# Performance work log

Hardware: AMD Instinct MI355X
Metric: run time of the kernel (lower is better)

Reference implementation:

```python
import math
import jax, jax.numpy as jnp
import numpy as np

B = 1024
D = 384
Q = 65536
TOPK = 128
HARD_W = 2.0
TEMP_START = 0.2
TEMP_END = 0.05
WARMUP = 10


def _temperature(epoch):
    # curriculum cosine decay (epoch is a Python int)
    if epoch >= WARMUP:
        return TEMP_END
    progress = epoch / max(1, WARMUP)
    return TEMP_END + 0.5 * (TEMP_START - TEMP_END) * (1.0 + math.cos(math.pi * progress))


def _normalize(x):
    # F.normalize: x / max(||x||, eps)
    n = jnp.linalg.norm(x, axis=-1, keepdims=True)
    return x / jnp.maximum(n, 1e-12)


def _hard_neg_reweight(logits):
    # logits: [B, N]; labels = arange(B) (diagonal positives)
    b = logits.shape[0]
    rows = jnp.arange(b)
    neg_logits = logits.at[rows, rows].set(-jnp.inf)      # mask positives
    _, hard_idx = jax.lax.top_k(neg_logits, TOPK)          # [B, TOPK] hardest negatives
    weights = jnp.ones_like(logits)
    weights = weights.at[rows[:, None], hard_idx].set(HARD_W)
    weights = weights.at[rows, rows].set(1.0)
    return logits * weights


def _cross_entropy_diag(logits):
    b = logits.shape[0]
    logp = jax.nn.log_softmax(logits, axis=-1)
    return -jnp.mean(logp[jnp.arange(b), jnp.arange(b)])


def setup_inputs() -> dict:
    key = jax.random.key(0)
    k1, k2, k3, k4 = jax.random.split(key, 4)
    rgb_feat = jax.random.normal(k1, (B, D), dtype=jnp.float32)
    ir_feat = jax.random.normal(k2, (B, D), dtype=jnp.float32)
    rgb_queue = _normalize(jax.random.normal(k3, (Q, D), dtype=jnp.float32))
    ir_queue = _normalize(jax.random.normal(k4, (Q, D), dtype=jnp.float32))
    return {"rgb_feat": rgb_feat, "ir_feat": ir_feat,
            "rgb_queue": rgb_queue, "ir_queue": ir_queue, "epoch": 0}


def reference(rgb_feat, ir_feat, rgb_queue, ir_queue, epoch):
    temp = _temperature(epoch)
    rgb_z = _normalize(rgb_feat.astype(jnp.float32))
    ir_z = _normalize(ir_feat.astype(jnp.float32))
    ir_all = jnp.concatenate([ir_z, ir_queue], axis=0)    # [B+Q, D]
    rgb_all = jnp.concatenate([rgb_z, rgb_queue], axis=0)
    logits_r2i = (rgb_z @ ir_all.T) / temp                # [B, B+Q]
    logits_i2r = (ir_z @ rgb_all.T) / temp
    logits_r2i = _hard_neg_reweight(logits_r2i)
    logits_i2r = _hard_neg_reweight(logits_i2r)
    return 0.5 * (_cross_entropy_diag(logits_r2i) + _cross_entropy_diag(logits_i2r))
```

## Files before the change

### kernel.cpp

```cpp
#include <hip/hip_runtime.h>
#include <hip/hip_bf16.h>

#define B_    1024
#define D_    384
#define Q_    65536
#define N_    66560
#define TOPK_ 128

#define NBIN_ 4096
#define CAP_  2048

typedef __bf16 bf16x8 __attribute__((ext_vector_type(8)));
typedef float  f32x4  __attribute__((ext_vector_type(4)));
typedef unsigned short u16;
typedef u16 u16x8 __attribute__((ext_vector_type(8)));

__device__ __forceinline__ unsigned short f2bf(float x) {
  unsigned int u = __float_as_uint(x);
  unsigned int r = (u + 0x7fffu + ((u >> 16) & 1u)) >> 16;
  return (unsigned short)r;
}

__device__ __forceinline__ void gld_lds16(const void* g, void* l) {
  __builtin_amdgcn_global_load_lds(
      (__attribute__((address_space(1))) void*)(g),
      (__attribute__((address_space(3))) void*)(l), 16, 0, 0);
}

__device__ __forceinline__ unsigned int bf2key(unsigned int u) {
  return u ^ ((u & 0x8000u) ? 0xFFFFu : 0x8000u);
}

__global__ __launch_bounds__(64) void k_normalize(
    const float* __restrict__ rgb, const float* __restrict__ ir,
    const int* __restrict__ ep,
    u16* __restrict__ zrA, u16* __restrict__ ziA,
    u16* __restrict__ zrU, u16* __restrict__ ziU)
{
  int r = blockIdx.x & (B_ - 1);
  bool isIr = blockIdx.x >= B_;
  const float* src = (isIr ? ir : rgb) + (size_t)r * D_;
  u16* dA = (isIr ? ziA : zrA) + (size_t)r * D_;
  u16* dU = (isIr ? ziU : zrU) + (size_t)r * D_;
  int t = threadIdx.x;
  float x[6]; float ss = 0.f;
  #pragma unroll
  for (int k = 0; k < 6; ++k) { x[k] = src[t + 64*k]; ss += x[k]*x[k]; }
  #pragma unroll
  for (int off = 32; off > 0; off >>= 1) ss += __shfl_down(ss, off);
  ss = __shfl(ss, 0);
  float inv = 1.0f / fmaxf(sqrtf(ss), 1e-12f);

  int e = ep[0];
  float temp;
  if (e >= 10) temp = 0.05f;
  else {
    float p = (float)e * 0.1f;
    temp = 0.05f + 0.075f * (1.0f + cosf(3.14159265358979323846f * p));
  }
  float itemp = 1.0f / temp;

  #pragma unroll
  for (int k = 0; k < 6; ++k) {
    float z = x[k] * inv;
    dU[t + 64*k] = f2bf(z);
    dA[t + 64*k] = f2bf(z * itemp);
  }
}

__global__ __launch_bounds__(256) void k_build_ball(
    const u16* __restrict__ zU, const float* __restrict__ queue,
    u16* __restrict__ ball)
{
  size_t i = ((size_t)blockIdx.x * 256 + threadIdx.x) * 8;
  const size_t zElems = (size_t)B_ * D_;
  if (i < zElems) {
    *(uint4*)(ball + i) = *(const uint4*)(zU + i);
  } else {
    const float* q = queue + (i - zElems);
    float4 a = *(const float4*)q;
    float4 b = *(const float4*)(q + 4);
    u16x8 o;
    o[0] = f2bf(a.x); o[1] = f2bf(a.y); o[2] = f2bf(a.z); o[3] = f2bf(a.w);
    o[4] = f2bf(b.x); o[5] = f2bf(b.y); o[6] = f2bf(b.z); o[7] = f2bf(b.w);
    *(u16x8*)(ball + i) = o;
  }
}

#define BK_ 64
__global__ __launch_bounds__(256) void k_gemm(
    const u16* __restrict__ A,
    const u16* __restrict__ ball,
    u16* __restrict__ C,
    float* __restrict__ diag,
    int r0, int mtiles)
{
  __shared__ u16 As[128 * BK_];
  __shared__ u16 Bs[128 * BK_];

  int bid = blockIdx.x;
  int nwg = gridDim.x;
  int cpx = nwg >> 3;
  int wgid = (bid & 7) * cpx + (bid >> 3);
  int nt = wgid / mtiles;
  int mt = wgid - nt * mtiles;

  const int tid  = threadIdx.x;
  const int wave = tid >> 6, lane = tid & 63;
  const int wm = wave >> 1, wn = wave & 1;
  const int mbase = mt * 128;
  const int nbase = nt * 128;
  const u16* Ab = A    + (size_t)(r0 + mbase) * D_;
  const u16* Bb = ball + (size_t)nbase * D_;

  f32x4 acc[4][4];
  #pragma unroll
  for (int m = 0; m < 4; ++m)
    #pragma unroll
    for (int n = 0; n < 4; ++n)
      #pragma unroll
      for (int r = 0; r < 4; ++r) acc[m][n][r] = 0.0f;

  for (int ks = 0; ks < D_; ks += BK_) {
    #pragma unroll
    for (int i = 0; i < 4; ++i) {
      int f = i * 256 + tid;
      int rr = f >> 3, c = f & 7;
      int koff = (((c * 16) ^ ((rr & 7) << 4)) >> 1);
      const u16* ga = Ab + (size_t)rr * D_ + ks + koff;
      const u16* gb = Bb + (size_t)rr * D_ + ks + koff;
      u16* la = As + (size_t)(i * 256 + wave * 64) * 8;
      u16* lb = Bs + (size_t)(i * 256 + wave * 64) * 8;
      gld_lds16(ga, la);
      gld_lds16(gb, lb);
    }
    __syncthreads();

    const int lr = lane & 15, lk = (lane >> 4) * 8;
    #pragma unroll
    for (int kk = 0; kk < BK_; kk += 32) {
      bf16x8 af[4], bq[4];
      const int kb = (kk + lk) * 2;
      #pragma unroll
      for (int m = 0; m < 4; ++m) {
        int row = wm*64 + m*16 + lr;
        af[m] = *(const bf16x8*)((const char*)As + row * 128 + (kb ^ ((row & 7) << 4)));
      }
      #pragma unroll
      for (int n = 0; n < 4; ++n) {
        int row = wn*64 + n*16 + lr;
        bq[n] = *(const bf16x8*)((const char*)Bs + row * 128 + (kb ^ ((row & 7) << 4)));
      }
      #pragma unroll
      for (int m = 0; m < 4; ++m)
        #pragma unroll
        for (int n = 0; n < 4; ++n)
          acc[m][n] = __builtin_amdgcn_mfma_f32_16x16x32_bf16(af[m], bq[n], acc[m][n], 0, 0, 0);
    }
    __syncthreads();
  }

  const int lr = lane & 15;
  const int rowq = (lane >> 4) * 4;
  #pragma unroll
  for (int m = 0; m < 4; ++m) {
    #pragma unroll
    for (int n = 0; n < 4; ++n) {
      int col = nbase + wn*64 + n*16 + lr;
      #pragma unroll
      for (int r = 0; r < 4; ++r) {
        int srow = mbase + wm*64 + m*16 + rowq + r;
        float x = acc[m][n][r];
        int grow = r0 + srow;
        if (col == grow) { diag[grow] = x; x = -60.0f; }
        C[(size_t)srow * N_ + col] = f2bf(x);
      }
    }
  }
}

__global__ __launch_bounds__(256) void k_select(
    const u16* __restrict__ C, const float* __restrict__ diag,
    float* __restrict__ rowloss, int r0)
{
  __shared__ unsigned int hist[NBIN_];
  __shared__ float vals[CAP_];
  __shared__ float fred[256];
  __shared__ unsigned int csum[256];
  __shared__ int sh_bstar, sh_above, sh_cnt;

  const int t = threadIdx.x;
  const int grow = r0 + blockIdx.x;
  const u16x8* p = (const u16x8*)(C + (size_t)blockIdx.x * N_);

  uint4* h4 = (uint4*)hist;
  #pragma unroll
  for (int i = 0; i < 4; ++i) h4[i * 256 + t] = make_uint4(0,0,0,0);
  if (t == 0) sh_cnt = 0;
  __syncthreads();

  float es0 = 0.f, es1 = 0.f;
  #pragma unroll 1
  for (int base = 0; base < 8192; base += 2048) {
    u16x8 v[8];
    #pragma unroll
    for (int j = 0; j < 8; ++j) v[j] = p[base + j * 256 + t];
    #pragma unroll
    for (int j = 0; j < 8; ++j) {
      #pragma unroll
      for (int e = 0; e < 8; ++e) {
        unsigned int u = (unsigned int)(unsigned short)v[j][e];
        atomicAdd(&hist[bf2key(u) >> 4], 1u);
        float ex = __expf(__uint_as_float(u << 16));
        if (j & 1) es1 += ex; else es0 += ex;
      }
    }
  }
  if (t < 128) {
    u16x8 v = p[8192 + t];
    #pragma unroll
    for (int e = 0; e < 8; ++e) {
      unsigned int u = (unsigned int)(unsigned short)v[e];
      atomicAdd(&hist[bf2key(u) >> 4], 1u);
      es0 += __expf(__uint_as_float(u << 16));
    }
  }
  float esum = es0 + es1;
  __syncthreads();

  unsigned int S = 0;
  #pragma unroll
  for (int i = 0; i < 16; ++i) S += hist[t * 16 + i];
  csum[t] = S;
  __syncthreads();

  unsigned int a = S;
  #pragma unroll
  for (int s = 1; s < 256; s <<= 1) {
    unsigned int add = (t + s < 256) ? csum[t + s] : 0u;
    __syncthreads();
    a += add; csum[t] = a;
    __syncthreads();
  }

  int above_chunk = (t < 255) ? (int)csum[t + 1] : 0;
  if (above_chunk < TOPK_ && above_chunk + (int)S >= TOPK_) {
    int cum = above_chunk;
    #pragma unroll 1
    for (int i = 15; i >= 0; --i) {
      int c = (int)hist[t * 16 + i];
      if (cum + c >= TOPK_) { sh_bstar = t * 16 + i; sh_above = cum; break; }
      cum += c;
    }
  }
  __syncthreads();
  const unsigned int bstar = (unsigned int)sh_bstar;
  const int A = sh_above;

  float delta = 0.f;
  #pragma unroll 1
  for (int base = 0; base < 8192; base += 2048) {
    u16x8 v[8];
    #pragma unroll
    for (int j = 0; j < 8; ++j) v[j] = p[base + j * 256 + t];
    #pragma unroll
    for (int j = 0; j < 8; ++j) {
      #pragma unroll
      for (int e = 0; e < 8; ++e) {
        unsigned int u = (unsigned int)(unsigned short)v[j][e];
        unsigned int bin = bf2key(u) >> 4;
        if (bin >= bstar) {
          float val = __uint_as_float(u << 16);
          if (bin > bstar) delta += __expf(2.f * val) - __expf(val);
          else { int s = atomicAdd(&sh_cnt, 1); if (s < CAP_) vals[s] = val; }
        }
      }
    }
  }
  if (t < 128) {
    u16x8 v = p[8192 + t];
    #pragma unroll
    for (int e = 0; e < 8; ++e) {
      unsigned int u = (unsigned int)(unsigned short)v[e];
      unsigned int bin = bf2key(u) >> 4;
      if (bin >= bstar) {
        float val = __uint_as_float(u << 16);
        if (bin > bstar) delta += __expf(2.f * val) - __expf(val);
        else { int s = atomicAdd(&sh_cnt, 1); if (s < CAP_) vals[s] = val; }
      }
    }
  }
  __syncthreads();

  int C2 = sh_cnt < CAP_ ? sh_cnt : CAP_;
  int need = TOPK_ - A;
  for (int i = t; i < C2; i += 256) {
    float v = vals[i];
    int g = 0;
    for (int k = 0; k < C2; ++k)
      g += (vals[k] > v) || (vals[k] == v && k < i);
    if (g < need) delta += __expf(2.f * v) - __expf(v);
  }

  fred[t] = esum + delta;
  __syncthreads();
  #pragma unroll
  for (int s = 128; s > 0; s >>= 1) { if (t < s) fred[t] += fred[t + s]; __syncthreads(); }

  if (t == 0) {
    float d = diag[grow];
    rowloss[grow] = logf(fred[0] + __expf(d)) - d;
  }
}

__global__ __launch_bounds__(256) void k_final(
    const float* __restrict__ rowloss, float* __restrict__ out)
{
  __shared__ float red[256];
  int t = threadIdx.x;
  float s = 0.f;
  for (int i = t; i < 2 * B_; i += 256) s += rowloss[i];
  red[t] = s;
  __syncthreads();
  for (int k = 128; k > 0; k >>= 1) { if (t < k) red[t] += red[t + k]; __syncthreads(); }
  if (t == 0) out[0] = red[0] * (1.0f / (2.0f * B_));
}

extern "C" void kernel_launch(void* const* d_in, const int* in_sizes, int n_in,
                              void* d_out, int out_size, void* d_ws, size_t ws_size,
                              hipStream_t stream)
{
  const float* rgb_feat = (const float*)d_in[0];
  const float* ir_feat  = (const float*)d_in[1];
  const float* rgb_q    = (const float*)d_in[2];
  const float* ir_q     = (const float*)d_in[3];
  const int*   epoch    = (const int*)d_in[4];

  char* ws = (char*)d_ws;
  size_t off = 0;
  auto alloc = [&](size_t bytes) -> char* {
    char* p = ws + off;
    off = (off + bytes + 255) & ~(size_t)255;
    return p;
  };

  u16* zrA = (u16*)alloc((size_t)B_ * D_ * 2);
  u16* ziA = (u16*)alloc((size_t)B_ * D_ * 2);
  u16* zrU = (u16*)alloc((size_t)B_ * D_ * 2);
  u16* ziU = (u16*)alloc((size_t)B_ * D_ * 2);
  float* diag    = (float*)alloc((size_t)2 * B_ * 4);
  float* rowloss = (float*)alloc((size_t)2 * B_ * 4);
  u16* ball = (u16*)alloc((size_t)N_ * D_ * 2);

  size_t avail = ws_size > off ? ws_size - off : 0;
  int SR = (int)(avail / ((size_t)N_ * 2));
  SR &= ~127;
  if (SR > B_) SR = B_;
  if (SR < 128) SR = 128;
  u16* slab = (u16*)(ws + off);

  k_normalize<<<dim3(2 * B_), dim3(64), 0, stream>>>(
      rgb_feat, ir_feat, epoch, zrA, ziA, zrU, ziU);

  for (int dir = 0; dir < 2; ++dir) {
    const u16*   Amat   = (dir == 0) ? zrA : ziA;
    const u16*   zOther = (dir == 0) ? ziU : zrU;
    const float* queue  = (dir == 0) ? ir_q : rgb_q;
    float* diagD = diag    + dir * B_;
    float* lossD = rowloss + dir * B_;

    k_build_ball<<<dim3((unsigned)((size_t)N_ * D_ / 8 / 256)), dim3(256), 0, stream>>>(
        zOther, queue, ball);

    for (int r0 = 0; r0 < B_; r0 += SR) {
      int cur = (B_ - r0) < SR ? (B_ - r0) : SR;
      int mtiles = cur / 128;
      int nwg = (N_ / 128) * mtiles;
      k_gemm<<<dim3(nwg), dim3(256), 0, stream>>>(
          Amat, ball, slab, diagD, r0, mtiles);
      k_select<<<dim3(cur), dim3(256), 0, stream>>>(slab, diagD, lossD, r0);
    }
  }

  k_final<<<dim3(1), dim3(256), 0, stream>>>(rowloss, (float*)d_out);
}
```

Baseline: 344.7 us.

## Fuse queue bf16 conversion into GEMM loads and coalesce C stores via LDS

Removes the separate ball-building kernel and has the GEMM read the fp32 queue directly, converting to bf16 while staging B tiles in LDS. The output tile is staged through a padded LDS buffer so global stores of the logits slab are 16-byte coalesced rows. This saves a full conversion pass and its buffer, but rereads fp32 queue data per row tile and replaces async direct-to-LDS loads with register-path loads for queue panels.

```diff
diff --git a/kernel.cpp b/kernel.cpp
--- a/kernel.cpp
+++ b/kernel.cpp
@@ -68,35 +68,19 @@
   }
 }
 
-__global__ __launch_bounds__(256) void k_build_ball(
-    const u16* __restrict__ zU, const float* __restrict__ queue,
-    u16* __restrict__ ball)
-{
-  size_t i = ((size_t)blockIdx.x * 256 + threadIdx.x) * 8;
-  const size_t zElems = (size_t)B_ * D_;
-  if (i < zElems) {
-    *(uint4*)(ball + i) = *(const uint4*)(zU + i);
-  } else {
-    const float* q = queue + (i - zElems);
-    float4 a = *(const float4*)q;
-    float4 b = *(const float4*)(q + 4);
-    u16x8 o;
-    o[0] = f2bf(a.x); o[1] = f2bf(a.y); o[2] = f2bf(a.z); o[3] = f2bf(a.w);
-    o[4] = f2bf(b.x); o[5] = f2bf(b.y); o[6] = f2bf(b.z); o[7] = f2bf(b.w);
-    *(u16x8*)(ball + i) = o;
-  }
-}
-
 #define BK_ 64
 __global__ __launch_bounds__(256) void k_gemm(
     const u16* __restrict__ A,
-    const u16* __restrict__ ball,
+    const u16* __restrict__ zOther,
+    const float* __restrict__ queue,
     u16* __restrict__ C,
     float* __restrict__ diag,
     int r0, int mtiles)
 {
-  __shared__ u16 As[128 * BK_];
-  __shared__ u16 Bs[128 * BK_];
+  __shared__ __align__(16) unsigned char smem[34816];
+  u16* As = (u16*)smem;
+  u16* Bs = (u16*)(smem + 16384);
+  u16* Ct = (u16*)smem;
 
   int bid = blockIdx.x;
   int nwg = gridDim.x;
@@ -110,8 +94,10 @@
   const int wm = wave >> 1, wn = wave & 1;
   const int mbase = mt * 128;
   const int nbase = nt * 128;
-  const u16* Ab = A    + (size_t)(r0 + mbase) * D_;
-  const u16* Bb = ball + (size_t)nbase * D_;
+  const bool qpanel = (nbase >= B_);
+  const u16*   Ab = A + (size_t)(r0 + mbase) * D_;
+  const u16*   Zb = zOther + (size_t)nbase * D_;
+  const float* Qb = queue + (size_t)(nbase - B_) * D_;
 
   f32x4 acc[4][4];
   #pragma unroll
@@ -127,12 +113,32 @@
       int f = i * 256 + tid;
       int rr = f >> 3, c = f & 7;
       int koff = (((c * 16) ^ ((rr & 7) << 4)) >> 1);
-      const u16* ga = Ab + (size_t)rr * D_ + ks + koff;
-      const u16* gb = Bb + (size_t)rr * D_ + ks + koff;
-      u16* la = As + (size_t)(i * 256 + wave * 64) * 8;
-      u16* lb = Bs + (size_t)(i * 256 + wave * 64) * 8;
-      gld_lds16(ga, la);
-      gld_lds16(gb, lb);
+      gld_lds16(Ab + (size_t)rr * D_ + ks + koff,
+                As + (size_t)f * 8);
+    }
+    if (qpanel) {
+      #pragma unroll
+      for (int i = 0; i < 4; ++i) {
+        int f = i * 256 + tid;
+        int rr = f >> 3, c = f & 7;
+        int koff = (((c * 16) ^ ((rr & 7) << 4)) >> 1);
+        const float* src = Qb + (size_t)rr * D_ + ks + koff;
+        float4 a = *(const float4*)src;
+        float4 b = *(const float4*)(src + 4);
+        u16x8 o;
+        o[0] = f2bf(a.x); o[1] = f2bf(a.y); o[2] = f2bf(a.z); o[3] = f2bf(a.w);
+        o[4] = f2bf(b.x); o[5] = f2bf(b.y); o[6] = f2bf(b.z); o[7] = f2bf(b.w);
+        *(u16x8*)(Bs + (size_t)f * 8) = o;
+      }
+    } else {
+      #pragma unroll
+      for (int i = 0; i < 4; ++i) {
+        int f = i * 256 + tid;
+        int rr = f >> 3, c = f & 7;
+        int koff = (((c * 16) ^ ((rr & 7) << 4)) >> 1);
+        gld_lds16(Zb + (size_t)rr * D_ + ks + koff,
+                  Bs + (size_t)f * 8);
+      }
     }
     __syncthreads();
 
@@ -166,16 +172,27 @@
   for (int m = 0; m < 4; ++m) {
     #pragma unroll
     for (int n = 0; n < 4; ++n) {
-      int col = nbase + wn*64 + n*16 + lr;
+      int lcol = wn*64 + n*16 + lr;
+      int gcol = nbase + lcol;
       #pragma unroll
       for (int r = 0; r < 4; ++r) {
-        int srow = mbase + wm*64 + m*16 + rowq + r;
+        int lrow = wm*64 + m*16 + rowq + r;
         float x = acc[m][n][r];
-        int grow = r0 + srow;
-        if (col == grow) { diag[grow] = x; x = -60.0f; }
-        C[(size_t)srow * N_ + col] = f2bf(x);
-      }
-    }
+        int grow = r0 + mbase + lrow;
+        if (gcol == grow) { diag[grow] = x; x = -60.0f; }
+        Ct[lrow * 136 + lcol] = f2bf(x);
+      }
+    }
+  }
+  __syncthreads();
+
+  int rrow = tid >> 4;
+  int cchunk = (tid & 15) * 8;
+  #pragma unroll
+  for (int pass = 0; pass < 8; ++pass) {
+    int row = pass * 16 + rrow;
+    u16x8 v = *(const u16x8*)(Ct + row * 136 + cchunk);
+    *(u16x8*)(C + (size_t)(mbase + row) * N_ + nbase + cchunk) = v;
   }
 }
 
@@ -350,7 +367,6 @@
   u16* ziU = (u16*)alloc((size_t)B_ * D_ * 2);
   float* diag    = (float*)alloc((size_t)2 * B_ * 4);
   float* rowloss = (float*)alloc((size_t)2 * B_ * 4);
-  u16* ball = (u16*)alloc((size_t)N_ * D_ * 2);
 
   size_t avail = ws_size > off ? ws_size - off : 0;
   int SR = (int)(avail / ((size_t)N_ * 2));
@@ -369,15 +385,12 @@
     float* diagD = diag    + dir * B_;
     float* lossD = rowloss + dir * B_;
 
-    k_build_ball<<<dim3((unsigned)((size_t)N_ * D_ / 8 / 256)), dim3(256), 0, stream>>>(
-        zOther, queue, ball);
-
     for (int r0 = 0; r0 < B_; r0 += SR) {
       int cur = (B_ - r0) < SR ? (B_ - r0) : SR;
       int mtiles = cur / 128;
       int nwg = (N_ / 128) * mtiles;
       k_gemm<<<dim3(nwg), dim3(256), 0, stream>>>(
-          Amat, ball, slab, diagD, r0, mtiles);
+          Amat, zOther, queue, slab, diagD, r0, mtiles);
       k_select<<<dim3(cur), dim3(256), 0, stream>>>(slab, diagD, lossD, r0);
     }
   }
```

New measurement: 332.0 us. 1.04x faster.

## Double-buffer GEMM LDS tiles and stage epilogue through LDS for coalesced stores

Applied to the files above, without the earlier changes.

The k_gemm main loop now keeps A/B tiles in two 32KB ping-pong LDS buffers and issues the global-to-LDS loads for the next K step before computing the current one, so memory latency overlaps with MFMA work and one barrier per step is removed. The epilogue writes the bf16 results into a padded LDS tile (row stride 136) and then stores 16-byte vectors per row, replacing the scattered 2-byte global stores. LDS use grows to 64KB per block, which may reduce occupancy.

```diff
diff --git a/kernel.cpp b/kernel.cpp
--- a/kernel.cpp
+++ b/kernel.cpp
@@ -88,6 +88,7 @@
 }
 
 #define BK_ 64
+#define NSTEP_ 6
 __global__ __launch_bounds__(256) void k_gemm(
     const u16* __restrict__ A,
     const u16* __restrict__ ball,
@@ -95,8 +96,10 @@
     float* __restrict__ diag,
     int r0, int mtiles)
 {
-  __shared__ u16 As[128 * BK_];
-  __shared__ u16 Bs[128 * BK_];
+  __shared__ __align__(16) unsigned char smem[65536];
+  u16* AsBuf[2] = { (u16*)smem,           (u16*)(smem + 32768) };
+  u16* BsBuf[2] = { (u16*)(smem + 16384), (u16*)(smem + 49152) };
+  u16* Ct = (u16*)smem;
 
   int bid = blockIdx.x;
   int nwg = gridDim.x;
@@ -113,6 +116,10 @@
   const u16* Ab = A    + (size_t)(r0 + mbase) * D_;
   const u16* Bb = ball + (size_t)nbase * D_;
 
+  const int rr0 = tid >> 3;
+  const int c0  = tid & 7;
+  const int koff = (((c0 * 16) ^ ((rr0 & 7) << 4)) >> 1);
+
   f32x4 acc[4][4];
   #pragma unroll
   for (int m = 0; m < 4; ++m)
@@ -121,22 +128,33 @@
       #pragma unroll
       for (int r = 0; r < 4; ++r) acc[m][n][r] = 0.0f;
 
-  for (int ks = 0; ks < D_; ks += BK_) {
-    #pragma unroll
-    for (int i = 0; i < 4; ++i) {
-      int f = i * 256 + tid;
-      int rr = f >> 3, c = f & 7;
-      int koff = (((c * 16) ^ ((rr & 7) << 4)) >> 1);
-      const u16* ga = Ab + (size_t)rr * D_ + ks + koff;
-      const u16* gb = Bb + (size_t)rr * D_ + ks + koff;
-      u16* la = As + (size_t)(i * 256 + wave * 64) * 8;
-      u16* lb = Bs + (size_t)(i * 256 + wave * 64) * 8;
-      gld_lds16(ga, la);
-      gld_lds16(gb, lb);
-    }
-    __syncthreads();
-
-    const int lr = lane & 15, lk = (lane >> 4) * 8;
+  const int lr = lane & 15, lk = (lane >> 4) * 8;
+
+  #pragma unroll
+  for (int i = 0; i < 4; ++i) {
+    int f = i * 256 + tid;
+    int rr = rr0 + i * 32;
+    gld_lds16(Ab + (size_t)rr * D_ + koff, AsBuf[0] + (size_t)f * 8);
+    gld_lds16(Bb + (size_t)rr * D_ + koff, BsBuf[0] + (size_t)f * 8);
+  }
+  __syncthreads();
+
+  #pragma unroll
+  for (int t = 0; t < NSTEP_; ++t) {
+    const int cur = t & 1;
+    u16* Ac = AsBuf[cur];
+    u16* Bc = BsBuf[cur];
+    if (t + 1 < NSTEP_) {
+      const int nxt = cur ^ 1;
+      const int ks = (t + 1) * BK_;
+      #pragma unroll
+      for (int i = 0; i < 4; ++i) {
+        int f = i * 256 + tid;
+        int rr = rr0 + i * 32;
+        gld_lds16(Ab + (size_t)rr * D_ + ks + koff, AsBuf[nxt] + (size_t)f * 8);
+        gld_lds16(Bb + (size_t)rr * D_ + ks + koff, BsBuf[nxt] + (size_t)f * 8);
+      }
+    }
     #pragma unroll
     for (int kk = 0; kk < BK_; kk += 32) {
       bf16x8 af[4], bq[4];
@@ -144,12 +162,12 @@
       #pragma unroll
       for (int m = 0; m < 4; ++m) {
         int row = wm*64 + m*16 + lr;
-        af[m] = *(const bf16x8*)((const char*)As + row * 128 + (kb ^ ((row & 7) << 4)));
+        af[m] = *(const bf16x8*)((const char*)Ac + row * 128 + (kb ^ ((row & 7) << 4)));
       }
       #pragma unroll
       for (int n = 0; n < 4; ++n) {
         int row = wn*64 + n*16 + lr;
-        bq[n] = *(const bf16x8*)((const char*)Bs + row * 128 + (kb ^ ((row & 7) << 4)));
+        bq[n] = *(const bf16x8*)((const char*)Bc + row * 128 + (kb ^ ((row & 7) << 4)));
       }
       #pragma unroll
       for (int m = 0; m < 4; ++m)
@@ -160,22 +178,32 @@
     __syncthreads();
   }
 
-  const int lr = lane & 15;
   const int rowq = (lane >> 4) * 4;
   #pragma unroll
   for (int m = 0; m < 4; ++m) {
     #pragma unroll
     for (int n = 0; n < 4; ++n) {
-      int col = nbase + wn*64 + n*16 + lr;
+      int lcol = wn*64 + n*16 + lr;
+      int gcol = nbase + lcol;
       #pragma unroll
       for (int r = 0; r < 4; ++r) {
-        int srow = mbase + wm*64 + m*16 + rowq + r;
+        int lrow = wm*64 + m*16 + rowq + r;
         float x = acc[m][n][r];
-        int grow = r0 + srow;
-        if (col == grow) { diag[grow] = x; x = -60.0f; }
-        C[(size_t)srow * N_ + col] = f2bf(x);
-      }
-    }
+        int grow = r0 + mbase + lrow;
+        if (gcol == grow) { diag[grow] = x; x = -60.0f; }
+        Ct[lrow * 136 + lcol] = f2bf(x);
+      }
+    }
+  }
+  __syncthreads();
+
+  int rrow = tid >> 4;
+  int cchunk = (tid & 15) * 8;
+  #pragma unroll
+  for (int pass = 0; pass < 8; ++pass) {
+    int row = pass * 16 + rrow;
+    u16x8 v = *(const u16x8*)(Ct + row * 136 + cchunk);
+    *(u16x8*)(C + (size_t)(mbase + row) * N_ + nbase + cchunk) = v;
   }
 }
 
```

Measured after the change: 336.6 us. 2.3% less time.
